# Kernel optimization log

Hardware: AMD Instinct MI355X
Metric: run time of the kernel (lower is better)

Reference implementation:

```python
import jax, jax.numpy as jnp
import numpy as np

B_TAIL = 3.0  # 'bins' arg = tail bound of the spline interval [-B, B]


def _rqs_forward(u, w, h, d):
    """Rational-quadratic spline (Durkan et al.) with linear (identity) tails.
    u: (batch, dim); w,h: (dim, K); d: (dim, K-1). Returns x (batch, dim), logdet (batch,)."""
    dim, K = w.shape
    two_b = 2.0 * B_TAIL

    widths = jax.nn.softmax(w, axis=-1) * two_b                      # (dim, K)
    cum_w = jnp.concatenate(
        [jnp.full((dim, 1), -B_TAIL, u.dtype), -B_TAIL + jnp.cumsum(widths, axis=-1)],
        axis=-1)                                                     # (dim, K+1) knot x-positions
    cum_w = cum_w.at[:, -1].set(B_TAIL)

    heights = jax.nn.softmax(h, axis=-1) * two_b                     # (dim, K)
    cum_h = jnp.concatenate(
        [jnp.full((dim, 1), -B_TAIL, u.dtype), -B_TAIL + jnp.cumsum(heights, axis=-1)],
        axis=-1)                                                     # (dim, K+1) knot y-positions
    cum_h = cum_h.at[:, -1].set(B_TAIL)

    ones = jnp.ones((dim, 1), u.dtype)
    derivs = jnp.concatenate([ones, jax.nn.softplus(d), ones], axis=-1)  # (dim, K+1)

    inside = (u >= -B_TAIL) & (u <= B_TAIL)
    uc = jnp.clip(u, -B_TAIL, B_TAIL)

    # bin search: count interior knots <= uc  -> bin index in [0, K-1]
    idx = jnp.sum(uc[:, :, None] >= cum_w[None, :, 1:-1], axis=-1)   # (batch, dim) int32

    didx = jnp.arange(dim)[None, :]                                  # (1, dim)
    xk  = cum_w[didx, idx]
    wk  = widths[didx, idx]
    yk  = cum_h[didx, idx]
    hk  = heights[didx, idx]
    dk  = derivs[didx, idx]
    dk1 = derivs[didx, idx + 1]

    delta = hk / wk                                                  # bin slope
    theta = (uc - xk) / wk
    t1m = theta * (1.0 - theta)
    denom = delta + (dk + dk1 - 2.0 * delta) * t1m
    num = hk * (delta * theta * theta + dk * t1m)
    x_in = yk + num / denom

    ld_num = delta * delta * (dk1 * theta * theta + 2.0 * delta * t1m
                              + dk * (1.0 - theta) * (1.0 - theta))
    ld_in = jnp.log(ld_num) - 2.0 * jnp.log(denom)

    x = jnp.where(inside, x_in, u)          # identity linear tails
    ld = jnp.where(inside, ld_in, 0.0)
    return x, jnp.sum(ld, axis=-1)


def setup_inputs() -> dict:
    key = jax.random.key(0)
    ku, kw, kh, kd = jax.random.split(key, 4)
    batch, dim, K = 131072, 256, 5
    u = jax.random.normal(ku, (batch, dim), dtype=jnp.float32)
    w = jax.random.uniform(kw, (dim, K), dtype=jnp.float32, minval=-0.5, maxval=0.5)
    h = jax.random.uniform(kh, (dim, K), dtype=jnp.float32, minval=-0.5, maxval=0.5)
    d = jax.random.uniform(kd, (dim, K - 1), dtype=jnp.float32, minval=-0.5, maxval=0.5)
    return {"u": u, "w": w, "h": h, "d": d}


def reference(u, w, h, d):
    return _rqs_forward(u, w, h, d)
```

## Files before the change

### kernel.cpp

```cpp
#include <hip/hip_runtime.h>
#include <math.h>

#define BATCH 131072
#define DIM 256
#define NK 5
#define BT 3.0f

__global__ __launch_bounds__(256, 4) void rqs_kernel(
    const float* __restrict__ u,
    const float* __restrict__ wp,
    const float* __restrict__ hp,
    const float* __restrict__ dp,
    float* __restrict__ x_out,
    float* __restrict__ ld_out)
{
    __shared__ float tab[26 * DIM];
    const int tid = threadIdx.x;

    {
        const int dm = tid;
        const int sp = ((dm & 3) << 6) | (dm >> 2);
        float v[NK];
        float mx, sum, scale, c;

        mx = -1e30f;
        #pragma unroll
        for (int k = 0; k < NK; k++) { v[k] = wp[dm * NK + k]; mx = fmaxf(mx, v[k]); }
        sum = 0.f;
        #pragma unroll
        for (int k = 0; k < NK; k++) { v[k] = expf(v[k] - mx); sum += v[k]; }
        scale = 6.0f / sum;
        c = -BT;
        #pragma unroll
        for (int k = 0; k < NK; k++) {
            float wid = v[k] * scale;
            tab[k * DIM + sp]       = c;
            tab[(5 + k) * DIM + sp] = 1.0f / wid;
            c += wid;
        }

        mx = -1e30f;
        #pragma unroll
        for (int k = 0; k < NK; k++) { v[k] = hp[dm * NK + k]; mx = fmaxf(mx, v[k]); }
        sum = 0.f;
        #pragma unroll
        for (int k = 0; k < NK; k++) { v[k] = expf(v[k] - mx); sum += v[k]; }
        scale = 6.0f / sum;
        c = -BT;
        #pragma unroll
        for (int k = 0; k < NK; k++) {
            float hei = v[k] * scale;
            tab[(10 + k) * DIM + sp] = c;
            tab[(15 + k) * DIM + sp] = hei;
            c += hei;
        }

        tab[20 * DIM + sp] = 1.0f;
        #pragma unroll
        for (int k = 0; k < 4; k++)
            tab[(21 + k) * DIM + sp] = log1pf(expf(dp[dm * 4 + k]));
        tab[25 * DIM + sp] = 1.0f;
    }
    __syncthreads();

    const int lane = tid & 63;
    const int wv   = tid >> 6;

    float kn[4][4];
    #pragma unroll
    for (int j = 0; j < 4; j++) {
        const int sp = (j << 6) | lane;
        #pragma unroll
        for (int i = 0; i < 4; i++)
            kn[j][i] = tab[(i + 1) * DIM + sp];
    }

    const int gw = (blockIdx.x << 2) | wv;
    const int nw = gridDim.x << 2;

    for (int row = gw; row < BATCH; row += nw) {
        const float4 uv = reinterpret_cast<const float4*>(u + (size_t)row * DIM)[lane];
        float uin[4] = {uv.x, uv.y, uv.z, uv.w};
        float xo[4];
        float ldsum = 0.f;
        #pragma unroll
        for (int j = 0; j < 4; j++) {
            float uval = uin[j];
            float uc = fminf(fmaxf(uval, -BT), BT);
            bool inside = (uval >= -BT) && (uval <= BT);
            int idx = 0;
            idx += (uc >= kn[j][0]);
            idx += (uc >= kn[j][1]);
            idx += (uc >= kn[j][2]);
            idx += (uc >= kn[j][3]);
            const int a = idx * DIM + ((j << 6) | lane);
            float xk  = tab[a];
            float iw  = tab[a + 5 * DIM];
            float yk  = tab[a + 10 * DIM];
            float hk  = tab[a + 15 * DIM];
            float dk  = tab[a + 20 * DIM];
            float dk1 = tab[a + 21 * DIM];

            float delta = hk * iw;
            float theta = (uc - xk) * iw;
            float omt   = 1.0f - theta;
            float t1m   = theta * omt;
            float th2   = theta * theta;
            float denom = delta + (dk + dk1 - 2.0f * delta) * t1m;
            float inv_d = __fdividef(1.0f, denom);
            float num   = hk * (delta * th2 + dk * t1m);
            float x_in  = yk + num * inv_d;
            float ldn   = (delta * delta) *
                          (dk1 * th2 + 2.0f * delta * t1m + dk * omt * omt);
            float ld    = __logf(ldn * inv_d * inv_d);

            xo[j] = inside ? x_in : uval;
            ldsum += inside ? ld : 0.0f;
        }
        reinterpret_cast<float4*>(x_out + (size_t)row * DIM)[lane] =
            make_float4(xo[0], xo[1], xo[2], xo[3]);

        #pragma unroll
        for (int off = 32; off > 0; off >>= 1)
            ldsum += __shfl_down(ldsum, off, 64);
        if (lane == 0) ld_out[row] = ldsum;
    }
}

extern "C" void kernel_launch(void* const* d_in, const int* in_sizes, int n_in,
                              void* d_out, int out_size, void* d_ws, size_t ws_size,
                              hipStream_t stream) {
    const float* u  = (const float*)d_in[0];
    const float* w  = (const float*)d_in[1];
    const float* h  = (const float*)d_in[2];
    const float* dd = (const float*)d_in[3];
    float* x  = (float*)d_out;
    float* ld = x + (size_t)BATCH * DIM;
    rqs_kernel<<<2048, 256, 0, stream>>>(u, w, h, dd, x, ld);
}
```

Measured before the change: 252.0 us.

## Pack spline tables into float4/float2 LDS, process two rows per wave

Replaces the 26-plane scalar LDS table with packed float4 (x knot, inverse width, y knot, height) and float2 (derivative pair) entries, so six scalar LDS reads per element become two vector reads. Global access changes from one float4 per lane to strided scalar loads, and each wave now handles two rows per iteration with the shuffle reductions interleaved. Outputs use nontemporal stores and the occupancy hint rises to 5 blocks. The wider LDS reads may cause bank conflicts, and more loads in flight per wave raise register pressure.

```diff
diff --git a/kernel.cpp b/kernel.cpp
--- a/kernel.cpp
+++ b/kernel.cpp
@@ -6,7 +6,7 @@
 #define NK 5
 #define BT 3.0f
 
-__global__ __launch_bounds__(256, 4) void rqs_kernel(
+__global__ __launch_bounds__(256, 5) void rqs_kernel(
     const float* __restrict__ u,
     const float* __restrict__ wp,
     const float* __restrict__ hp,
@@ -14,14 +14,15 @@
     float* __restrict__ x_out,
     float* __restrict__ ld_out)
 {
-    __shared__ float tab[26 * DIM];
+    __shared__ float4 tabA[NK * DIM];
+    __shared__ float2 tabB[NK * DIM];
     const int tid = threadIdx.x;
 
     {
         const int dm = tid;
-        const int sp = ((dm & 3) << 6) | (dm >> 2);
         float v[NK];
         float mx, sum, scale, c;
+        float wid[NK], xpos[NK], hei[NK], ypos[NK], dv[NK + 1];
 
         mx = -1e30f;
         #pragma unroll
@@ -32,12 +33,7 @@
         scale = 6.0f / sum;
         c = -BT;
         #pragma unroll
-        for (int k = 0; k < NK; k++) {
-            float wid = v[k] * scale;
-            tab[k * DIM + sp]       = c;
-            tab[(5 + k) * DIM + sp] = 1.0f / wid;
-            c += wid;
-        }
+        for (int k = 0; k < NK; k++) { wid[k] = v[k] * scale; xpos[k] = c; c += wid[k]; }
 
         mx = -1e30f;
         #pragma unroll
@@ -48,18 +44,17 @@
         scale = 6.0f / sum;
         c = -BT;
         #pragma unroll
+        for (int k = 0; k < NK; k++) { hei[k] = v[k] * scale; ypos[k] = c; c += hei[k]; }
+
+        dv[0] = 1.0f; dv[NK] = 1.0f;
+        #pragma unroll
+        for (int k = 0; k < 4; k++) dv[1 + k] = log1pf(expf(dp[dm * 4 + k]));
+
+        #pragma unroll
         for (int k = 0; k < NK; k++) {
-            float hei = v[k] * scale;
-            tab[(10 + k) * DIM + sp] = c;
-            tab[(15 + k) * DIM + sp] = hei;
-            c += hei;
+            tabA[k * DIM + dm] = make_float4(xpos[k], 1.0f / wid[k], ypos[k], hei[k]);
+            tabB[k * DIM + dm] = make_float2(dv[k], dv[k + 1]);
         }
-
-        tab[20 * DIM + sp] = 1.0f;
-        #pragma unroll
-        for (int k = 0; k < 4; k++)
-            tab[(21 + k) * DIM + sp] = log1pf(expf(dp[dm * 4 + k]));
-        tab[25 * DIM + sp] = 1.0f;
     }
     __syncthreads();
 
@@ -69,61 +64,74 @@
     float kn[4][4];
     #pragma unroll
     for (int j = 0; j < 4; j++) {
-        const int sp = (j << 6) | lane;
         #pragma unroll
         for (int i = 0; i < 4; i++)
-            kn[j][i] = tab[(i + 1) * DIM + sp];
+            kn[j][i] = tabA[(i + 1) * DIM + lane + 64 * j].x;
     }
 
     const int gw = (blockIdx.x << 2) | wv;
     const int nw = gridDim.x << 2;
 
-    for (int row = gw; row < BATCH; row += nw) {
-        const float4 uv = reinterpret_cast<const float4*>(u + (size_t)row * DIM)[lane];
-        float uin[4] = {uv.x, uv.y, uv.z, uv.w};
-        float xo[4];
-        float ldsum = 0.f;
+    for (int base = gw * 2; base < BATCH; base += nw * 2) {
+        float uin[2][4];
         #pragma unroll
-        for (int j = 0; j < 4; j++) {
-            float uval = uin[j];
-            float uc = fminf(fmaxf(uval, -BT), BT);
-            bool inside = (uval >= -BT) && (uval <= BT);
-            int idx = 0;
-            idx += (uc >= kn[j][0]);
-            idx += (uc >= kn[j][1]);
-            idx += (uc >= kn[j][2]);
-            idx += (uc >= kn[j][3]);
-            const int a = idx * DIM + ((j << 6) | lane);
-            float xk  = tab[a];
-            float iw  = tab[a + 5 * DIM];
-            float yk  = tab[a + 10 * DIM];
-            float hk  = tab[a + 15 * DIM];
-            float dk  = tab[a + 20 * DIM];
-            float dk1 = tab[a + 21 * DIM];
+        for (int rr = 0; rr < 2; rr++) {
+            const float* up = u + (size_t)(base + rr) * DIM + lane;
+            #pragma unroll
+            for (int j = 0; j < 4; j++) uin[rr][j] = up[64 * j];
+        }
 
-            float delta = hk * iw;
-            float theta = (uc - xk) * iw;
-            float omt   = 1.0f - theta;
-            float t1m   = theta * omt;
-            float th2   = theta * theta;
-            float denom = delta + (dk + dk1 - 2.0f * delta) * t1m;
-            float inv_d = __fdividef(1.0f, denom);
-            float num   = hk * (delta * th2 + dk * t1m);
-            float x_in  = yk + num * inv_d;
-            float ldn   = (delta * delta) *
-                          (dk1 * th2 + 2.0f * delta * t1m + dk * omt * omt);
-            float ld    = __logf(ldn * inv_d * inv_d);
+        float ldsum[2] = {0.f, 0.f};
+        #pragma unroll
+        for (int rr = 0; rr < 2; rr++) {
+            float xo[4];
+            #pragma unroll
+            for (int j = 0; j < 4; j++) {
+                float uval = uin[rr][j];
+                float uc = fminf(fmaxf(uval, -BT), BT);
+                bool inside = (uval >= -BT) && (uval <= BT);
+                int idx = 0;
+                idx += (uc >= kn[j][0]);
+                idx += (uc >= kn[j][1]);
+                idx += (uc >= kn[j][2]);
+                idx += (uc >= kn[j][3]);
+                const int a = idx * DIM + lane + 64 * j;
+                float4 A  = tabA[a];
+                float2 Bv = tabB[a];
+                float xk = A.x, iw = A.y, yk = A.z, hk = A.w;
+                float dk = Bv.x, dk1 = Bv.y;
 
-            xo[j] = inside ? x_in : uval;
-            ldsum += inside ? ld : 0.0f;
+                float delta = hk * iw;
+                float theta = (uc - xk) * iw;
+                float omt   = 1.0f - theta;
+                float t1m   = theta * omt;
+                float th2   = theta * theta;
+                float denom = delta + (dk + dk1 - 2.0f * delta) * t1m;
+                float inv_d = __fdividef(1.0f, denom);
+                float num   = hk * (delta * th2 + dk * t1m);
+                float x_in  = yk + num * inv_d;
+                float ldn   = (delta * delta) *
+                              (dk1 * th2 + 2.0f * delta * t1m + dk * omt * omt);
+                float ld    = __logf(ldn * inv_d * inv_d);
+
+                xo[j] = inside ? x_in : uval;
+                ldsum[rr] += inside ? ld : 0.0f;
+            }
+            float* xp = x_out + (size_t)(base + rr) * DIM + lane;
+            #pragma unroll
+            for (int j = 0; j < 4; j++)
+                __builtin_nontemporal_store(xo[j], xp + 64 * j);
         }
-        reinterpret_cast<float4*>(x_out + (size_t)row * DIM)[lane] =
-            make_float4(xo[0], xo[1], xo[2], xo[3]);
 
         #pragma unroll
-        for (int off = 32; off > 0; off >>= 1)
-            ldsum += __shfl_down(ldsum, off, 64);
-        if (lane == 0) ld_out[row] = ldsum;
+        for (int off = 32; off > 0; off >>= 1) {
+            ldsum[0] += __shfl_down(ldsum[0], off, 64);
+            ldsum[1] += __shfl_down(ldsum[1], off, 64);
+        }
+        if (lane == 0) {
+            __builtin_nontemporal_store(ldsum[0], ld_out + base);
+            __builtin_nontemporal_store(ldsum[1], ld_out + base + 1);
+        }
     }
 }
 
```

Measured after the change: 246.5 us. -2.2%, faster.
